# Optimization experiments

Hardware: AMD Instinct MI355X
Metric: run time of the kernel (lower is better)

Reference implementation:

```python
import jax, jax.numpy as jnp
import numpy as np

N_BLOCKS = 7  # completed blocks; partial_block makes the N axis 8
B, L, D = 2, 4096, 2048


def setup_inputs() -> dict:
    key = jax.random.key(0)
    k1, k2, k3 = jax.random.split(key, 3)
    blocks = jax.random.normal(k1, (N_BLOCKS, B, L, D), dtype=jnp.float32)
    partial_block = jax.random.normal(k2, (B, L, D), dtype=jnp.float32)
    norm_scale = jnp.ones((D,), dtype=jnp.float32)
    proj = 0.02 * jax.random.normal(k3, (D,), dtype=jnp.float32)
    return {"blocks": blocks, "partial_block": partial_block,
            "norm_scale": norm_scale, "proj": proj}


def reference(blocks, partial_block, norm_scale, proj):
    # V: [N, B, L, D] = stack of completed blocks plus current partial sum
    V = jnp.concatenate([blocks, partial_block[None]], axis=0)
    # Per-(n,b,l) RMS normalization with learned scale (RMSNorm)
    rms = jnp.sqrt(jnp.mean(V * V, axis=-1, keepdims=True) + 1e-6)
    K = V / rms * norm_scale
    # Single learned-query attention score over the small N axis
    logits = jnp.einsum('d,nbld->nbl', proj, K)
    weights = jax.nn.softmax(logits, axis=0)
    # Weighted sum of unnormalized block states -> [B, L, D]
    return jnp.einsum('nbl,nbld->bld', weights, V)
```

## Files before the change

### kernel.cpp

```cpp
#include <hip/hip_runtime.h>
#include <stdint.h>

#define NB   8
#define DDIM 2048
#define BLK  256

__global__ __launch_bounds__(BLK) void attn_residual_kernel(
    const float* __restrict__ blocks,
    const float* __restrict__ partial,
    const float* __restrict__ scale,
    const float* __restrict__ proj,
    float*       __restrict__ out,
    int BL)
{
    const int bl = blockIdx.x;
    const int t  = threadIdx.x;
    const size_t row     = (size_t)bl * DDIM;
    const size_t nstride = (size_t)BL * DDIM;
    const int dA = t * 4;
    const int dB = t * 4 + 1024;

    const float4 prA = *(const float4*)(proj  + dA);
    const float4 prB = *(const float4*)(proj  + dB);
    const float4 scA = *(const float4*)(scale + dA);
    const float4 scB = *(const float4*)(scale + dB);
    const float4 pA = make_float4(prA.x*scA.x, prA.y*scA.y, prA.z*scA.z, prA.w*scA.w);
    const float4 pB = make_float4(prB.x*scB.x, prB.y*scB.y, prB.z*scB.z, prB.w*scB.w);

    float4 vA[NB], vB[NB];
    #pragma unroll
    for (int n = 0; n < NB - 1; ++n) {
        const float* src = blocks + (size_t)n * nstride + row;
        vA[n] = *(const float4*)(src + dA);
        vB[n] = *(const float4*)(src + dB);
    }
    vA[NB-1] = *(const float4*)(partial + row + dA);
    vB[NB-1] = *(const float4*)(partial + row + dB);

    float ss[NB], dt[NB];
    #pragma unroll
    for (int n = 0; n < NB; ++n) {
        float s = 0.f, d = 0.f;
        s = fmaf(vA[n].x, vA[n].x, s); s = fmaf(vA[n].y, vA[n].y, s);
        s = fmaf(vA[n].z, vA[n].z, s); s = fmaf(vA[n].w, vA[n].w, s);
        s = fmaf(vB[n].x, vB[n].x, s); s = fmaf(vB[n].y, vB[n].y, s);
        s = fmaf(vB[n].z, vB[n].z, s); s = fmaf(vB[n].w, vB[n].w, s);
        d = fmaf(pA.x, vA[n].x, d); d = fmaf(pA.y, vA[n].y, d);
        d = fmaf(pA.z, vA[n].z, d); d = fmaf(pA.w, vA[n].w, d);
        d = fmaf(pB.x, vB[n].x, d); d = fmaf(pB.y, vB[n].y, d);
        d = fmaf(pB.z, vB[n].z, d); d = fmaf(pB.w, vB[n].w, d);
        ss[n] = s; dt[n] = d;
    }

    #pragma unroll
    for (int n = 0; n < NB; ++n) {
        float a = ss[n], b = dt[n];
        #pragma unroll
        for (int off = 32; off > 0; off >>= 1) {
            a += __shfl_down(a, off, 64);
            b += __shfl_down(b, off, 64);
        }
        ss[n] = a; dt[n] = b;
    }

    __shared__ float red[4][2][NB];
    const int wave = t >> 6, lane = t & 63;
    if (lane == 0) {
        #pragma unroll
        for (int n = 0; n < NB; ++n) {
            red[wave][0][n] = ss[n];
            red[wave][1][n] = dt[n];
        }
    }
    __syncthreads();

    float w[NB];
    float m = -1e30f;
    #pragma unroll
    for (int n = 0; n < NB; ++n) {
        float s = red[0][0][n] + red[1][0][n] + red[2][0][n] + red[3][0][n];
        float d = red[0][1][n] + red[1][1][n] + red[2][1][n] + red[3][1][n];
        float rms = sqrtf(s * (1.0f / DDIM) + 1e-6f);
        float logit = d / rms;
        w[n] = logit;
        m = fmaxf(m, logit);
    }
    float denom = 0.f;
    #pragma unroll
    for (int n = 0; n < NB; ++n) {
        w[n] = __expf(w[n] - m);
        denom += w[n];
    }
    const float inv = 1.0f / denom;

    float4 oA = make_float4(0.f, 0.f, 0.f, 0.f);
    float4 oB = make_float4(0.f, 0.f, 0.f, 0.f);
    #pragma unroll
    for (int n = 0; n < NB; ++n) {
        const float wn = w[n];
        oA.x = fmaf(wn, vA[n].x, oA.x); oA.y = fmaf(wn, vA[n].y, oA.y);
        oA.z = fmaf(wn, vA[n].z, oA.z); oA.w = fmaf(wn, vA[n].w, oA.w);
        oB.x = fmaf(wn, vB[n].x, oB.x); oB.y = fmaf(wn, vB[n].y, oB.y);
        oB.z = fmaf(wn, vB[n].z, oB.z); oB.w = fmaf(wn, vB[n].w, oB.w);
    }
    oA.x *= inv; oA.y *= inv; oA.z *= inv; oA.w *= inv;
    oB.x *= inv; oB.y *= inv; oB.z *= inv; oB.w *= inv;
    *(float4*)(out + row + dA) = oA;
    *(float4*)(out + row + dB) = oB;
}

extern "C" void kernel_launch(void* const* d_in, const int* in_sizes, int n_in,
                              void* d_out, int out_size, void* d_ws, size_t ws_size,
                              hipStream_t stream) {
    const float* blocks  = (const float*)d_in[0];
    const float* partial = (const float*)d_in[1];
    const float* scale   = (const float*)d_in[2];
    const float* proj    = (const float*)d_in[3];
    float* out = (float*)d_out;

    const int BL = in_sizes[1] / DDIM;
    attn_residual_kernel<<<dim3(BL), dim3(BLK), 0, stream>>>(
        blocks, partial, scale, proj, out, BL);
}
```

Measured before the change: 657.6 us.

## Map one row per wavefront and stream blocks twice with nontemporal output

Each row is now handled by a single 64-lane wavefront instead of a 256-thread block. This removes the LDS reduction and the block barrier, and leaves only xor shuffles within the wave. The kernel no longer keeps all eight block vectors in registers. It first accumulates squared sums and dot products, then re-reads the inputs in a second pass to form the weighted sum, using nontemporal loads and stores. A 48 KB dynamic shared allocation that is never used is added, apparently to cap occupancy so each row's data stays cached for the second pass. The cost is roughly double the global read traffic if that re-read misses cache.

```diff
diff --git a/kernel.cpp b/kernel.cpp
--- a/kernel.cpp
+++ b/kernel.cpp
@@ -4,6 +4,8 @@
 #define NB   8
 #define DDIM 2048
 #define BLK  256
+
+typedef float v4f __attribute__((ext_vector_type(4)));
 
 __global__ __launch_bounds__(BLK) void attn_residual_kernel(
     const float* __restrict__ blocks,
@@ -13,100 +15,76 @@
     float*       __restrict__ out,
     int BL)
 {
-    const int bl = blockIdx.x;
-    const int t  = threadIdx.x;
-    const size_t row     = (size_t)bl * DDIM;
+    const int lane  = threadIdx.x & 63;
+    const int wv    = threadIdx.x >> 6;
+    const int rowid = (blockIdx.x << 2) | wv;
+    const size_t row     = (size_t)rowid * DDIM;
     const size_t nstride = (size_t)BL * DDIM;
-    const int dA = t * 4;
-    const int dB = t * 4 + 1024;
 
-    const float4 prA = *(const float4*)(proj  + dA);
-    const float4 prB = *(const float4*)(proj  + dB);
-    const float4 scA = *(const float4*)(scale + dA);
-    const float4 scB = *(const float4*)(scale + dB);
-    const float4 pA = make_float4(prA.x*scA.x, prA.y*scA.y, prA.z*scA.z, prA.w*scA.w);
-    const float4 pB = make_float4(prB.x*scB.x, prB.y*scB.y, prB.z*scB.z, prB.w*scB.w);
-
-    float4 vA[NB], vB[NB];
+    const float* bases[NB];
     #pragma unroll
-    for (int n = 0; n < NB - 1; ++n) {
-        const float* src = blocks + (size_t)n * nstride + row;
-        vA[n] = *(const float4*)(src + dA);
-        vB[n] = *(const float4*)(src + dB);
-    }
-    vA[NB-1] = *(const float4*)(partial + row + dA);
-    vB[NB-1] = *(const float4*)(partial + row + dB);
+    for (int n = 0; n < NB - 1; ++n) bases[n] = blocks + (size_t)n * nstride + row;
+    bases[NB - 1] = partial + row;
 
     float ss[NB], dt[NB];
     #pragma unroll
-    for (int n = 0; n < NB; ++n) {
-        float s = 0.f, d = 0.f;
-        s = fmaf(vA[n].x, vA[n].x, s); s = fmaf(vA[n].y, vA[n].y, s);
-        s = fmaf(vA[n].z, vA[n].z, s); s = fmaf(vA[n].w, vA[n].w, s);
-        s = fmaf(vB[n].x, vB[n].x, s); s = fmaf(vB[n].y, vB[n].y, s);
-        s = fmaf(vB[n].z, vB[n].z, s); s = fmaf(vB[n].w, vB[n].w, s);
-        d = fmaf(pA.x, vA[n].x, d); d = fmaf(pA.y, vA[n].y, d);
-        d = fmaf(pA.z, vA[n].z, d); d = fmaf(pA.w, vA[n].w, d);
-        d = fmaf(pB.x, vB[n].x, d); d = fmaf(pB.y, vB[n].y, d);
-        d = fmaf(pB.z, vB[n].z, d); d = fmaf(pB.w, vB[n].w, d);
-        ss[n] = s; dt[n] = d;
+    for (int n = 0; n < NB; ++n) { ss[n] = 0.f; dt[n] = 0.f; }
+
+    const int d0 = lane << 2;
+
+    #pragma unroll 2
+    for (int j = 0; j < 8; ++j) {
+        const int d = (j << 8) + d0;
+        const v4f pr = *(const v4f*)(proj  + d);
+        const v4f sc = *(const v4f*)(scale + d);
+        const v4f p  = pr * sc;
+        #pragma unroll
+        for (int n = 0; n < NB; ++n) {
+            const v4f x = *(const v4f*)(bases[n] + d);
+            ss[n] = fmaf(x.x, x.x, fmaf(x.y, x.y, fmaf(x.z, x.z, fmaf(x.w, x.w, ss[n]))));
+            dt[n] = fmaf(p.x, x.x, fmaf(p.y, x.y, fmaf(p.z, x.z, fmaf(p.w, x.w, dt[n]))));
+        }
     }
 
     #pragma unroll
     for (int n = 0; n < NB; ++n) {
         float a = ss[n], b = dt[n];
         #pragma unroll
-        for (int off = 32; off > 0; off >>= 1) {
-            a += __shfl_down(a, off, 64);
-            b += __shfl_down(b, off, 64);
+        for (int off = 1; off < 64; off <<= 1) {
+            a += __shfl_xor(a, off, 64);
+            b += __shfl_xor(b, off, 64);
         }
         ss[n] = a; dt[n] = b;
     }
 
-    __shared__ float red[4][2][NB];
-    const int wave = t >> 6, lane = t & 63;
-    if (lane == 0) {
-        #pragma unroll
-        for (int n = 0; n < NB; ++n) {
-            red[wave][0][n] = ss[n];
-            red[wave][1][n] = dt[n];
-        }
-    }
-    __syncthreads();
-
-    float w[NB];
-    float m = -1e30f;
+    float w[NB], m = -1e30f;
     #pragma unroll
     for (int n = 0; n < NB; ++n) {
-        float s = red[0][0][n] + red[1][0][n] + red[2][0][n] + red[3][0][n];
-        float d = red[0][1][n] + red[1][1][n] + red[2][1][n] + red[3][1][n];
-        float rms = sqrtf(s * (1.0f / DDIM) + 1e-6f);
-        float logit = d / rms;
-        w[n] = logit;
-        m = fmaxf(m, logit);
+        const float rms = sqrtf(ss[n] * (1.0f / DDIM) + 1e-6f);
+        w[n] = dt[n] / rms;
+        m = fmaxf(m, w[n]);
     }
     float denom = 0.f;
     #pragma unroll
-    for (int n = 0; n < NB; ++n) {
-        w[n] = __expf(w[n] - m);
-        denom += w[n];
+    for (int n = 0; n < NB; ++n) { w[n] = __expf(w[n] - m); denom += w[n]; }
+    const float inv = 1.0f / denom;
+    #pragma unroll
+    for (int n = 0; n < NB; ++n) w[n] *= inv;
+
+    #pragma unroll 2
+    for (int j = 0; j < 8; ++j) {
+        const int d = (j << 8) + d0;
+        v4f o = {0.f, 0.f, 0.f, 0.f};
+        #pragma unroll
+        for (int n = 0; n < NB; ++n) {
+            const v4f x = __builtin_nontemporal_load((const v4f*)(bases[n] + d));
+            o.x = fmaf(w[n], x.x, o.x);
+            o.y = fmaf(w[n], x.y, o.y);
+            o.z = fmaf(w[n], x.z, o.z);
+            o.w = fmaf(w[n], x.w, o.w);
+        }
+        __builtin_nontemporal_store(o, (v4f*)(out + row + d));
     }
-    const float inv = 1.0f / denom;
-
-    float4 oA = make_float4(0.f, 0.f, 0.f, 0.f);
-    float4 oB = make_float4(0.f, 0.f, 0.f, 0.f);
-    #pragma unroll
-    for (int n = 0; n < NB; ++n) {
-        const float wn = w[n];
-        oA.x = fmaf(wn, vA[n].x, oA.x); oA.y = fmaf(wn, vA[n].y, oA.y);
-        oA.z = fmaf(wn, vA[n].z, oA.z); oA.w = fmaf(wn, vA[n].w, oA.w);
-        oB.x = fmaf(wn, vB[n].x, oB.x); oB.y = fmaf(wn, vB[n].y, oB.y);
-        oB.z = fmaf(wn, vB[n].z, oB.z); oB.w = fmaf(wn, vB[n].w, oB.w);
-    }
-    oA.x *= inv; oA.y *= inv; oA.z *= inv; oA.w *= inv;
-    oB.x *= inv; oB.y *= inv; oB.z *= inv; oB.w *= inv;
-    *(float4*)(out + row + dA) = oA;
-    *(float4*)(out + row + dB) = oB;
 }
 
 extern "C" void kernel_launch(void* const* d_in, const int* in_sizes, int n_in,
@@ -119,6 +97,6 @@
     float* out = (float*)d_out;
 
     const int BL = in_sizes[1] / DDIM;
-    attn_residual_kernel<<<dim3(BL), dim3(BLK), 0, stream>>>(
+    attn_residual_kernel<<<dim3(BL / 4), dim3(BLK), 48 * 1024, stream>>>(
         blocks, partial, scale, proj, out, BL);
 }
```

After: 698.3 us. 1.06x slower.
